# Kernel optimization log

Hardware: AMD Instinct MI355X
Metric: run time of the kernel (lower is better)

## Reference

```python
import jax, jax.numpy as jnp
import numpy as np

H = 128  # hidden size


def _gru_scan(xp, w_hh, b_hh):
    # xp: [T, B, 3H] precomputed input projections, PyTorch gate order (r, z, n)
    h0 = jnp.zeros((xp.shape[1], H), xp.dtype)
    def step(h, xt):
        g = h @ w_hh.T + b_hh
        xr, xz, xn = jnp.split(xt, 3, axis=-1)
        hr, hz, hn = jnp.split(g, 3, axis=-1)
        r = jax.nn.sigmoid(xr + hr)
        z = jax.nn.sigmoid(xz + hz)
        n = jnp.tanh(xn + r * hn)
        h = (1.0 - z) * n + z * h
        return h, h
    h_T, ys = jax.lax.scan(step, h0, xp)
    return h_T, ys


def _bidir_layer(x, wi_f, wh_f, bi_f, bh_f, wi_b, wh_b, bi_b, bh_b):
    # x: [T, B, D_in] time-major; returns concat outputs [T, B, 2H] and final hiddens
    h_f, y_f = _gru_scan(x @ wi_f.T + bi_f, wh_f, bh_f)
    h_b, y_b = _gru_scan(x[::-1] @ wi_b.T + bi_b, wh_b, bh_b)
    return jnp.concatenate([y_f, y_b[::-1]], axis=-1), h_f, h_b


def setup_inputs() -> dict:
    key = jax.random.key(0)
    ks = iter(jax.random.split(key, 40))
    scale = 1.0 / np.sqrt(H)
    def p(shape):
        return jax.random.normal(next(ks), shape, jnp.float32) * scale
    inp = {"x": jax.random.normal(next(ks), (512, 512, 4), jnp.float32)}
    for l, din in ((0, 4), (1, 2 * H)):
        for d in ("f", "b"):
            inp[f"w_ih_l{l}{d}"] = p((3 * H, din))
            inp[f"w_hh_l{l}{d}"] = p((3 * H, H))
            inp[f"b_ih_l{l}{d}"] = p((3 * H,))
            inp[f"b_hh_l{l}{d}"] = p((3 * H,))
    inp["fc1_w"] = p((H, 2 * H)); inp["fc1_b"] = p((H,))
    inp["fc2_w"] = p((2, H));     inp["fc2_b"] = p((2,))
    return inp


def reference(x, w_ih_l0f, w_hh_l0f, b_ih_l0f, b_hh_l0f,
              w_ih_l0b, w_hh_l0b, b_ih_l0b, b_hh_l0b,
              w_ih_l1f, w_hh_l1f, b_ih_l1f, b_hh_l1f,
              w_ih_l1b, w_hh_l1b, b_ih_l1b, b_hh_l1b,
              fc1_w, fc1_b, fc2_w, fc2_b):
    xt = jnp.transpose(x, (1, 0, 2))  # [T, B, F] time-major
    y0, _, _ = _bidir_layer(xt, w_ih_l0f, w_hh_l0f, b_ih_l0f, b_hh_l0f,
                            w_ih_l0b, w_hh_l0b, b_ih_l0b, b_hh_l0b)
    # dropout between layers is identity in eval mode
    _, h_f, h_b = _bidir_layer(y0, w_ih_l1f, w_hh_l1f, b_ih_l1f, b_hh_l1f,
                               w_ih_l1b, w_hh_l1b, b_ih_l1b, b_hh_l1b)
    h = jnp.concatenate([h_f, h_b], axis=-1)  # [B, 2H] = last-layer final hiddens, fwd then bwd
    h = jax.nn.relu(h @ fc1_w.T + fc1_b)
    return h @ fc2_w.T + fc2_b  # [B, num_classes]
```

## Files before the change

kernel.cpp:

```cpp
#include <hip/hip_runtime.h>
#include <stdint.h>


#define Tt 512
#define Bb 512
#define THREADS 512

using s16x8 = __attribute__((ext_vector_type(8))) short;
using f32x4 = __attribute__((ext_vector_type(4))) float;

#define MF(a, b, c) __builtin_amdgcn_mfma_f32_16x16x32_bf16((a), (b), (c), 0, 0, 0)

__device__ __forceinline__ unsigned short f2bf(float f) {
    union { float f; unsigned int u; } v; v.f = f;
    unsigned int u = v.u;
    u += 0x7fffu + ((u >> 16) & 1u);
    return (unsigned short)(u >> 16);
}
__device__ __forceinline__ float bf2f(unsigned short h) {
    union { unsigned int u; float f; } v; v.u = ((unsigned int)h) << 16;
    return v.f;
}

__device__ __forceinline__ float fsig(float x) {
    return __builtin_amdgcn_rcpf(1.0f + __expf(-x));
}
__device__ __forceinline__ float ftanh(float x) {
    return 2.0f * __builtin_amdgcn_rcpf(1.0f + __expf(-2.0f * x)) - 1.0f;
}

#define WG_BARRIER() asm volatile("s_waitcnt lgkmcnt(0)\n\ts_barrier" ::: "memory")

__global__ void w_prep(const float* __restrict__ wihf, const float* __restrict__ wihb,
                       const float* __restrict__ bihf, const float* __restrict__ bihb,
                       unsigned short* __restrict__ wcat, float* __restrict__ bcat)
{
    const int n = blockIdx.x;
    const int k = threadIdx.x;
    const float* src = (n < 384) ? &wihf[(size_t)n * 256] : &wihb[(size_t)(n - 384) * 256];
    wcat[(size_t)n * 256 + k] = f2bf(src[k]);
    if (k == 0) bcat[n] = (n < 384) ? bihf[n] : bihb[n - 384];
}

__global__ __launch_bounds__(THREADS) void l1_step(
    const unsigned short* __restrict__ y0,
    const unsigned short* __restrict__ wcat,
    const float* __restrict__ bcat,
    const unsigned short* __restrict__ gx_rd,
    unsigned short* __restrict__ gx_wr,
    const float* __restrict__ whh_f, const float* __restrict__ bhh_f,
    const float* __restrict__ whh_b, const float* __restrict__ bhh_b,
    float* __restrict__ hstate,
    int CT, int kgemm, int nscan, int first)
{
    const int bid  = blockIdx.x;
    const int tid  = threadIdx.x;
    const int wave = tid >> 6;
    const int lane = tid & 63;
    const int lcol = lane & 15;
    const int quad = lane >> 4;

    __shared__ __align__(16) unsigned short lA[128][136];
    __shared__ __align__(16) unsigned short lB[128][136];
    __shared__ __align__(16) unsigned short lds_h[2][16][136];

    if (bid >= nscan) {
        int gb = bid - nscan;
        const int nt = gb % 3;  gb /= 3;
        const int bt = gb & 3;  gb >>= 2;
        const int sl = gb % CT;
        const int dir = gb / CT;
        const int s  = kgemm * CT + sl;
        const int t  = dir ? (511 - s) : s;
        const int bb = bt << 7;

        const unsigned short* Abase = y0 + ((size_t)t * 512 + bb) * 256;
        const unsigned short* Bbase = wcat + ((size_t)dir * 384 + nt * 128) * 256;

        const int r0 = (wave >> 2) * 64;
        const int c0 = (wave & 3) * 32;

        f32x4 acc[4][2];
#pragma unroll
        for (int ti = 0; ti < 4; ++ti)
#pragma unroll
            for (int tj = 0; tj < 2; ++tj) acc[ti][tj] = {0.f, 0.f, 0.f, 0.f};

        const int rstg = tid >> 4;
        const int cstg = (tid & 15) * 8;

#pragma unroll
        for (int kh = 0; kh < 2; ++kh) {
            if (kh) __syncthreads();
#pragma unroll
            for (int it = 0; it < 4; ++it) {
                const int r = it * 32 + rstg;
                *(ulonglong2*)&lA[r][cstg] =
                    *(const ulonglong2*)&Abase[(size_t)r * 256 + kh * 128 + cstg];
                *(ulonglong2*)&lB[r][cstg] =
                    *(const ulonglong2*)&Bbase[(size_t)r * 256 + kh * 128 + cstg];
            }
            __syncthreads();

#pragma unroll
            for (int kk = 0; kk < 4; ++kk) {
                s16x8 af[4], bfv[2];
#pragma unroll
                for (int ti = 0; ti < 4; ++ti)
                    af[ti] = *(const s16x8*)&lA[r0 + ti * 16 + lcol][kk * 32 + quad * 8];
#pragma unroll
                for (int tj = 0; tj < 2; ++tj)
                    bfv[tj] = *(const s16x8*)&lB[c0 + tj * 16 + lcol][kk * 32 + quad * 8];
#pragma unroll
                for (int ti = 0; ti < 4; ++ti)
#pragma unroll
                    for (int tj = 0; tj < 2; ++tj)
                        acc[ti][tj] = MF(af[ti], bfv[tj], acc[ti][tj]);
            }
        }

        float bias[2];
#pragma unroll
        for (int tj = 0; tj < 2; ++tj)
            bias[tj] = bcat[dir * 384 + nt * 128 + c0 + tj * 16 + lcol];

        __syncthreads();

        unsigned short* lC = &lA[0][0];
#pragma unroll
        for (int ti = 0; ti < 4; ++ti)
#pragma unroll
            for (int tj = 0; tj < 2; ++tj) {
                const int col = c0 + tj * 16 + lcol;
#pragma unroll
                for (int i = 0; i < 4; ++i)
                    lC[(size_t)(r0 + ti * 16 + 4 * quad + i) * 136 + col] =
                        f2bf(acc[ti][tj][i] + bias[tj]);
            }
        __syncthreads();

        unsigned short* ob = gx_wr + ((size_t)(dir * CT + sl) * 512 + bb) * 384 + nt * 128;
#pragma unroll
        for (int it = 0; it < 4; ++it) {
            const int r = it * 32 + rstg;
            *(ulonglong2*)&ob[(size_t)r * 384 + cstg] =
                *(const ulonglong2*)&lC[(size_t)r * 136 + cstg];
        }
        return;
    }

    const int dir   = bid >> 5;
    const int chunk = bid & 31;
    const int b0    = chunk * 16;
    const int c     = 16 * wave + lcol;

    const float* whh = dir ? whh_b : whh_f;
    const float* bhh = dir ? bhh_b : bhh_f;

    const float bhr = bhh[c];
    const float bhz = bhh[128 + c];
    const float bhn = bhh[256 + c];

    s16x8 bh[3][4];
#pragma unroll
    for (int p = 0; p < 3; ++p) {
        const int nrow = p * 128 + c;
#pragma unroll
        for (int kk = 0; kk < 4; ++kk) {
            const float* src = &whh[(size_t)nrow * 128 + kk * 32 + quad * 8];
            s16x8 f;
#pragma unroll
            for (int j = 0; j < 8; ++j) f[j] = (short)f2bf(src[j]);
            bh[p][kk] = f;
        }
    }

    const unsigned short* gbase = gx_rd + (size_t)dir * CT * 512 * 384;
    auto loadGX = [&](unsigned short (&G)[12], int sl) {
        const unsigned short* gp = gbase + ((size_t)sl * 512 + b0 + 4 * quad) * 384;
#pragma unroll
        for (int g = 0; g < 3; ++g)
#pragma unroll
            for (int i = 0; i < 4; ++i)
                G[g * 4 + i] = gp[(size_t)i * 384 + g * 128 + c];
    };
    unsigned short G0[12], G1[12];
    loadGX(G0, 0);
    loadGX(G1, 1);

    float hreg[4];
    const int gb2 = tid >> 5;
    const int j0  = (tid & 31) * 4;
    if (first) {
#pragma unroll
        for (int i = 0; i < 4; ++i) hreg[i] = 0.f;
        ushort4 z4; z4.x = 0; z4.y = 0; z4.z = 0; z4.w = 0;
        *(ushort4*)&lds_h[0][gb2][j0] = z4;
    } else {
#pragma unroll
        for (int i = 0; i < 4; ++i)
            hreg[i] = hstate[(size_t)(b0 + 4 * quad + i) * 256 + dir * 128 + c];
        ushort4 hv;
        hv.x = f2bf(hstate[(size_t)(b0 + gb2) * 256 + dir * 128 + j0 + 0]);
        hv.y = f2bf(hstate[(size_t)(b0 + gb2) * 256 + dir * 128 + j0 + 1]);
        hv.z = f2bf(hstate[(size_t)(b0 + gb2) * 256 + dir * 128 + j0 + 2]);
        hv.w = f2bf(hstate[(size_t)(b0 + gb2) * 256 + dir * 128 + j0 + 3]);
        *(ushort4*)&lds_h[0][gb2][j0] = hv;
    }
    __syncthreads();

#define L1C_STEP(S, PAR, G)                                                    \
    do {                                                                       \
        const s16x8 a0 = *(const s16x8*)&lds_h[PAR][lcol][0  + quad * 8];      \
        const s16x8 a1 = *(const s16x8*)&lds_h[PAR][lcol][32 + quad * 8];      \
        const s16x8 a2 = *(const s16x8*)&lds_h[PAR][lcol][64 + quad * 8];      \
        const s16x8 a3 = *(const s16x8*)&lds_h[PAR][lcol][96 + quad * 8];      \
        f32x4 rA = {bhr, bhr, bhr, bhr}, rB = {0.f, 0.f, 0.f, 0.f};            \
        f32x4 zA = {bhz, bhz, bhz, bhz}, zB = {0.f, 0.f, 0.f, 0.f};            \
        f32x4 nA = {bhn, bhn, bhn, bhn}, nB = {0.f, 0.f, 0.f, 0.f};            \
        rA = MF(a0, bh[0][0], rA); zA = MF(a0, bh[1][0], zA);                  \
        nA = MF(a0, bh[2][0], nA);                                             \
        rB = MF(a1, bh[0][1], rB); zB = MF(a1, bh[1][1], zB);                  \
        nB = MF(a1, bh[2][1], nB);                                             \
        rA = MF(a2, bh[0][2], rA); zA = MF(a2, bh[1][2], zA);                  \
        nA = MF(a2, bh[2][2], nA);                                             \
        rB = MF(a3, bh[0][3], rB); zB = MF(a3, bh[1][3], zB);                  \
        nB = MF(a3, bh[2][3], nB);                                             \
        _Pragma("unroll")                                                      \
        for (int i = 0; i < 4; ++i) {                                          \
            const float r = fsig(rA[i] + rB[i] + bf2f(G[i]));                  \
            const float z = fsig(zA[i] + zB[i] + bf2f(G[4 + i]));              \
            const float n = ftanh(bf2f(G[8 + i]) + r * (nA[i] + nB[i]));       \
            hreg[i] = (1.0f - z) * n + z * hreg[i];                            \
            lds_h[PAR ^ 1][4 * quad + i][c] = f2bf(hreg[i]);                   \
        }                                                                      \
        if ((S) < CT - 2) {                                                    \
            loadGX(G, (S) + 2);                                                \
        } else if ((S) == CT - 1) {                                            \
            _Pragma("unroll")                                                  \
            for (int i = 0; i < 4; ++i)                                        \
                hstate[(size_t)(b0 + 4 * quad + i) * 256 + dir * 128 + c] =    \
                    hreg[i];                                                   \
        }                                                                      \
        WG_BARRIER();                                                          \
    } while (0)

    for (int sl = 0; sl < CT; sl += 2) {
        L1C_STEP(sl,     0, G0);
        L1C_STEP(sl + 1, 1, G1);
    }
#undef L1C_STEP
}

__global__ __launch_bounds__(THREADS, 1) void gru_l1(
    const unsigned short* __restrict__ y0,
    const float* __restrict__ wih_f, const float* __restrict__ whh_f,
    const float* __restrict__ bih_f, const float* __restrict__ bhh_f,
    const float* __restrict__ wih_b, const float* __restrict__ whh_b,
    const float* __restrict__ bih_b, const float* __restrict__ bhh_b,
    float* __restrict__ finals)
{
    const int tid  = threadIdx.x;
    const int wave = tid >> 6;
    const int lane = tid & 63;
    const int lcol = lane & 15;
    const int quad = lane >> 4;
    const int dir   = blockIdx.x >> 5;
    const int b0    = (blockIdx.x & 31) * 16;
    const int c     = 16 * wave + lcol;

    const float* wih = dir ? wih_b : wih_f;
    const float* whh = dir ? whh_b : whh_f;
    const float* bih = dir ? bih_b : bih_f;
    const float* bhh = dir ? bhh_b : bhh_f;

    __shared__ __align__(16) unsigned short lds_h[2][16][136];

    const float br  = bih[c]       + bhh[c];
    const float bz  = bih[128 + c] + bhh[128 + c];
    const float bnx = bih[256 + c];
    const float bnh = bhh[256 + c];

    s16x8 bh[3][4];
    s16x8 bx[3][8];
#pragma unroll
    for (int p = 0; p < 3; ++p) {
        const int nrow = p * 128 + c;
#pragma unroll
        for (int kk = 0; kk < 4; ++kk) {
            const float* src = &whh[(size_t)nrow * 128 + kk * 32 + quad * 8];
            s16x8 f;
#pragma unroll
            for (int j = 0; j < 8; ++j) f[j] = (short)f2bf(src[j]);
            bh[p][kk] = f;
        }
#pragma unroll
        for (int kk = 0; kk < 8; ++kk) {
            const float* src = &wih[(size_t)nrow * 256 + kk * 32 + quad * 8];
            s16x8 f;
#pragma unroll
            for (int j = 0; j < 8; ++j) f[j] = (short)f2bf(src[j]);
            bx[p][kk] = f;
        }
    }

    auto loadP = [&](s16x8 (&P)[8], int t) {
        const unsigned short* pb = y0 + ((size_t)t * Bb + b0 + lcol) * 256 + quad * 8;
#pragma unroll
        for (int kk = 0; kk < 8; ++kk) P[kk] = *(const s16x8*)(pb + kk * 32);
    };
    s16x8 P0[8], P1[8];
    loadP(P0, dir ? 511 : 0);
    loadP(P1, dir ? 510 : 1);

    f32x4 accr = {br, br, br, br};
    f32x4 accz = {bz, bz, bz, bz};
    f32x4 accnx = {bnx, bnx, bnx, bnx};
#pragma unroll
    for (int kk = 0; kk < 8; ++kk) {
        accr  = MF(P0[kk], bx[0][kk], accr);
        accz  = MF(P0[kk], bx[1][kk], accz);
        accnx = MF(P0[kk], bx[2][kk], accnx);
    }
    loadP(P0, dir ? 509 : 2);

    float hreg[4] = {0.f, 0.f, 0.f, 0.f};
    for (int idx = tid; idx < 2 * 16 * 136; idx += THREADS)
        ((unsigned short*)lds_h)[idx] = 0;
    __syncthreads();

#define L1_STEP(S, PAR, PN)                                                    \
    do {                                                                       \
        const s16x8 a0 = *(const s16x8*)&lds_h[PAR][lcol][0  + quad * 8];      \
        const s16x8 a1 = *(const s16x8*)&lds_h[PAR][lcol][32 + quad * 8];      \
        const s16x8 a2 = *(const s16x8*)&lds_h[PAR][lcol][64 + quad * 8];      \
        const s16x8 a3 = *(const s16x8*)&lds_h[PAR][lcol][96 + quad * 8];      \
        f32x4 acchn = {bnh, bnh, bnh, bnh};                                    \
        accr = MF(a0, bh[0][0], accr); accz = MF(a0, bh[1][0], accz);          \
        acchn = MF(a0, bh[2][0], acchn);                                       \
        accr = MF(a1, bh[0][1], accr); accz = MF(a1, bh[1][1], accz);          \
        acchn = MF(a1, bh[2][1], acchn);                                       \
        accr = MF(a2, bh[0][2], accr); accz = MF(a2, bh[1][2], accz);          \
        acchn = MF(a2, bh[2][2], acchn);                                       \
        accr = MF(a3, bh[0][3], accr); accz = MF(a3, bh[1][3], accz);          \
        acchn = MF(a3, bh[2][3], acchn);                                       \
        _Pragma("unroll")                                                      \
        for (int i = 0; i < 4; ++i) {                                          \
            const float r = fsig(accr[i]);                                     \
            const float z = fsig(accz[i]);                                     \
            const float n = ftanh(accnx[i] + r * acchn[i]);                    \
            hreg[i] = (1.0f - z) * n + z * hreg[i];                            \
            lds_h[PAR ^ 1][4 * quad + i][c] = f2bf(hreg[i]);                   \
        }                                                                      \
        if ((S) < 511) {                                                       \
            accr = {br, br, br, br}; accz = {bz, bz, bz, bz};                  \
            accnx = {bnx, bnx, bnx, bnx};                                      \
            _Pragma("unroll")                                                  \
            for (int kk = 0; kk < 8; ++kk) {                                   \
                accr  = MF(PN[kk], bx[0][kk], accr);                           \
                accz  = MF(PN[kk], bx[1][kk], accz);                           \
                accnx = MF(PN[kk], bx[2][kk], accnx);                          \
            }                                                                  \
            int sp = (S) + 3; if (sp > 511) sp = 511;                          \
            loadP(PN, dir ? (511 - sp) : sp);                                  \
        } else {                                                               \
            _Pragma("unroll")                                                  \
            for (int i = 0; i < 4; ++i)                                        \
                finals[(size_t)(b0 + 4 * quad + i) * 256 + dir * 128 + c] =    \
                    hreg[i];                                                   \
        }                                                                      \
        WG_BARRIER();                                                          \
    } while (0)

    for (int s = 0; s < Tt; s += 2) {
        L1_STEP(s,     0, P1);
        L1_STEP(s + 1, 1, P0);
    }
#undef L1_STEP
}

__global__ __launch_bounds__(THREADS, 1) void gru_l0(
    const float* __restrict__ x,
    const float* __restrict__ wih_f, const float* __restrict__ whh_f,
    const float* __restrict__ bih_f, const float* __restrict__ bhh_f,
    const float* __restrict__ wih_b, const float* __restrict__ whh_b,
    const float* __restrict__ bih_b, const float* __restrict__ bhh_b,
    unsigned short* __restrict__ y0)
{
    const int tid  = threadIdx.x;
    const int wave = tid >> 6;
    const int lane = tid & 63;
    const int lcol = lane & 15;
    const int quad = lane >> 4;
    const int dir   = blockIdx.x >> 5;
    const int b0    = (blockIdx.x & 31) * 16;
    const int c     = 16 * wave + lcol;

    const float* wih = dir ? wih_b : wih_f;
    const float* whh = dir ? whh_b : whh_f;
    const float* bih = dir ? bih_b : bih_f;
    const float* bhh = dir ? bhh_b : bhh_f;

    __shared__ __align__(16) unsigned short lds_h[2][16][136];

    const float brs  = bih[c]       + bhh[c];
    const float bzs  = bih[128 + c] + bhh[128 + c];
    const float bnxs = bih[256 + c];
    const float bnh  = bhh[256 + c];

    float wr[4], wz[4], wn[4];
#pragma unroll
    for (int f = 0; f < 4; ++f) {
        wr[f] = wih[(c)       * 4 + f];
        wz[f] = wih[(128 + c) * 4 + f];
        wn[f] = wih[(256 + c) * 4 + f];
    }

    s16x8 bh[3][4];
#pragma unroll
    for (int p = 0; p < 3; ++p) {
        const int nrow = p * 128 + c;
#pragma unroll
        for (int kk = 0; kk < 4; ++kk) {
            const float* src = &whh[(size_t)nrow * 128 + kk * 32 + quad * 8];
            s16x8 f;
#pragma unroll
            for (int j = 0; j < 8; ++j) f[j] = (short)f2bf(src[j]);
            bh[p][kk] = f;
        }
    }

    auto loadX = [&](float4 (&X)[4], int t) {
#pragma unroll
        for (int i = 0; i < 4; ++i)
            X[i] = *(const float4*)&x[((size_t)(b0 + 4 * quad + i) * Tt + t) * 4];
    };
    float4 X0[4], X1[4];
    loadX(X0, dir ? 511 : 0);
    loadX(X1, dir ? 510 : 1);

    float xpr[4], xpz[4], xpn[4];
#pragma unroll
    for (int i = 0; i < 4; ++i) {
        xpr[i] = brs  + X0[i].x * wr[0] + X0[i].y * wr[1] + X0[i].z * wr[2] + X0[i].w * wr[3];
        xpz[i] = bzs  + X0[i].x * wz[0] + X0[i].y * wz[1] + X0[i].z * wz[2] + X0[i].w * wz[3];
        xpn[i] = bnxs + X0[i].x * wn[0] + X0[i].y * wn[1] + X0[i].z * wn[2] + X0[i].w * wn[3];
    }
    loadX(X0, dir ? 509 : 2);

    float hreg[4] = {0.f, 0.f, 0.f, 0.f};
    for (int idx = tid; idx < 2 * 16 * 136; idx += THREADS)
        ((unsigned short*)lds_h)[idx] = 0;
    __syncthreads();

    const int orow = tid >> 5;
    const int oc4  = (tid & 31) * 4;

#define L0_STEP(S, PAR, XN)                                                    \
    do {                                                                       \
        const int t = dir ? (511 - (S)) : (S);                                 \
        const s16x8 a0 = *(const s16x8*)&lds_h[PAR][lcol][0  + quad * 8];      \
        const s16x8 a1 = *(const s16x8*)&lds_h[PAR][lcol][32 + quad * 8];      \
        const s16x8 a2 = *(const s16x8*)&lds_h[PAR][lcol][64 + quad * 8];      \
        const s16x8 a3 = *(const s16x8*)&lds_h[PAR][lcol][96 + quad * 8];      \
        f32x4 accr  = {xpr[0], xpr[1], xpr[2], xpr[3]};                        \
        f32x4 accz  = {xpz[0], xpz[1], xpz[2], xpz[3]};                        \
        f32x4 acchn = {bnh, bnh, bnh, bnh};                                    \
        accr = MF(a0, bh[0][0], accr); accz = MF(a0, bh[1][0], accz);          \
        acchn = MF(a0, bh[2][0], acchn);                                       \
        accr = MF(a1, bh[0][1], accr); accz = MF(a1, bh[1][1], accz);          \
        acchn = MF(a1, bh[2][1], acchn);                                       \
        accr = MF(a2, bh[0][2], accr); accz = MF(a2, bh[1][2], accz);          \
        acchn = MF(a2, bh[2][2], acchn);                                       \
        accr = MF(a3, bh[0][3], accr); accz = MF(a3, bh[1][3], accz);          \
        acchn = MF(a3, bh[2][3], acchn);                                       \
        _Pragma("unroll")                                                      \
        for (int i = 0; i < 4; ++i) {                                          \
            const float r = fsig(accr[i]);                                     \
            const float z = fsig(accz[i]);                                     \
            const float n = ftanh(xpn[i] + r * acchn[i]);                      \
            hreg[i] = (1.0f - z) * n + z * hreg[i];                            \
            lds_h[PAR ^ 1][4 * quad + i][c] = f2bf(hreg[i]);                   \
        }                                                                      \
        if ((S) < 511) {                                                       \
            _Pragma("unroll")                                                  \
            for (int i = 0; i < 4; ++i) {                                      \
                xpr[i] = brs  + XN[i].x * wr[0] + XN[i].y * wr[1]              \
                              + XN[i].z * wr[2] + XN[i].w * wr[3];             \
                xpz[i] = bzs  + XN[i].x * wz[0] + XN[i].y * wz[1]              \
                              + XN[i].z * wz[2] + XN[i].w * wz[3];             \
                xpn[i] = bnxs + XN[i].x * wn[0] + XN[i].y * wn[1]              \
                              + XN[i].z * wn[2] + XN[i].w * wn[3];             \
            }                                                                  \
            int sp = (S) + 3; if (sp > 511) sp = 511;                          \
            loadX(XN, dir ? (511 - sp) : sp);                                  \
        }                                                                      \
        WG_BARRIER();                                                          \
        {                                                                      \
            const ushort4 hv4 = *(const ushort4*)&lds_h[PAR ^ 1][orow][oc4];   \
            *(ushort4*)&y0[((size_t)t * Bb + b0 + orow) * 256 + dir * 128 +    \
                           oc4] = hv4;                                         \
        }                                                                      \
    } while (0)

    for (int s = 0; s < Tt; s += 2) {
        L0_STEP(s,     0, X1);
        L0_STEP(s + 1, 1, X0);
    }
#undef L0_STEP
}

__global__ __launch_bounds__(128) void fc_head(
    const float* __restrict__ finals,
    const float* __restrict__ fc1w, const float* __restrict__ fc1b,
    const float* __restrict__ fc2w, const float* __restrict__ fc2b,
    float* __restrict__ out)
{
    __shared__ float s_in[256];
    __shared__ float s_h1[128];
    const int b = blockIdx.x, tid = threadIdx.x;
    s_in[tid]       = finals[(size_t)b * 256 + tid];
    s_in[tid + 128] = finals[(size_t)b * 256 + 128 + tid];
    __syncthreads();
    float acc = fc1b[tid];
    const float* wrow = &fc1w[tid * 256];
#pragma unroll 8
    for (int i = 0; i < 256; ++i) acc += s_in[i] * wrow[i];
    s_h1[tid] = fmaxf(acc, 0.0f);
    __syncthreads();
    if (tid < 2) {
        float a = fc2b[tid];
        const float* w2 = &fc2w[tid * 128];
#pragma unroll 8
        for (int i = 0; i < 128; ++i) a += s_h1[i] * w2[i];
        out[b * 2 + tid] = a;
    }
}

extern "C" void kernel_launch(void* const* d_in, const int* in_sizes, int n_in,
                              void* d_out, int out_size, void* d_ws, size_t ws_size,
                              hipStream_t stream) {
    const float* x      = (const float*)d_in[0];
    const float* wih0f  = (const float*)d_in[1];
    const float* whh0f  = (const float*)d_in[2];
    const float* bih0f  = (const float*)d_in[3];
    const float* bhh0f  = (const float*)d_in[4];
    const float* wih0b  = (const float*)d_in[5];
    const float* whh0b  = (const float*)d_in[6];
    const float* bih0b  = (const float*)d_in[7];
    const float* bhh0b  = (const float*)d_in[8];
    const float* wih1f  = (const float*)d_in[9];
    const float* whh1f  = (const float*)d_in[10];
    const float* bih1f  = (const float*)d_in[11];
    const float* bhh1f  = (const float*)d_in[12];
    const float* wih1b  = (const float*)d_in[13];
    const float* whh1b  = (const float*)d_in[14];
    const float* bih1b  = (const float*)d_in[15];
    const float* bhh1b  = (const float*)d_in[16];
    const float* fc1w   = (const float*)d_in[17];
    const float* fc1b   = (const float*)d_in[18];
    const float* fc2w   = (const float*)d_in[19];
    const float* fc2b   = (const float*)d_in[20];

    const size_t Y0SZ = 134217728ull;
    const size_t HSSZ = 524288ull;
    const size_t WCSZ = 393216ull;
    const size_t BCSZ = 3072ull;
    const size_t GX_PER_SL = 786432ull;
    const size_t BASE = Y0SZ + HSSZ + WCSZ + BCSZ;

    unsigned short* y0 = (unsigned short*)d_ws;
    float*  hstate = (float*)((char*)d_ws + Y0SZ);
    unsigned short* wcat = (unsigned short*)((char*)d_ws + Y0SZ + HSSZ);
    float*  bcat   = (float*)((char*)d_ws + Y0SZ + HSSZ + WCSZ);
    unsigned short* gx0 = (unsigned short*)((char*)d_ws + BASE);
    float* out = (float*)d_out;

    const int cts[6] = {128, 64, 32, 16, 8, 4};
    int CT = 0, fused = 0;
    for (int i = 0; i < 6; ++i)
        if (BASE + 2ull * cts[i] * GX_PER_SL <= ws_size) { CT = cts[i]; fused = 1; break; }
    if (!CT)
        for (int i = 0; i < 6; ++i)
            if (BASE + (size_t)cts[i] * GX_PER_SL <= ws_size) { CT = cts[i]; break; }

    if (CT > 0) {
        unsigned short* gxb[2];
        gxb[0] = gx0;
        gxb[1] = fused ? (unsigned short*)((char*)gx0 + (size_t)CT * GX_PER_SL) : gx0;

        w_prep<<<dim3(768), dim3(256), 0, stream>>>(wih1f, wih1b, bih1f, bih1b, wcat, bcat);
        gru_l0<<<dim3(64), dim3(THREADS), 0, stream>>>(
            x, wih0f, whh0f, bih0f, bhh0f, wih0b, whh0b, bih0b, bhh0b, y0);
        const int n = Tt / CT;
        if (fused) {
            l1_step<<<dim3(24 * CT), dim3(THREADS), 0, stream>>>(
                y0, wcat, bcat, gxb[0], gxb[0],
                whh1f, bhh1f, whh1b, bhh1b, hstate, CT, 0, 0, 1);
            for (int k = 0; k < n; ++k) {
                const int ng = (k + 1 < n) ? 24 * CT : 0;
                l1_step<<<dim3(64 + ng), dim3(THREADS), 0, stream>>>(
                    y0, wcat, bcat, gxb[k & 1], gxb[(k + 1) & 1],
                    whh1f, bhh1f, whh1b, bhh1b, hstate, CT, k + 1, 64, (k == 0) ? 1 : 0);
            }
        } else {
            for (int k = 0; k < n; ++k) {
                l1_step<<<dim3(24 * CT), dim3(THREADS), 0, stream>>>(
                    y0, wcat, bcat, gxb[0], gxb[0],
                    whh1f, bhh1f, whh1b, bhh1b, hstate, CT, k, 0, 1);
                l1_step<<<dim3(64), dim3(THREADS), 0, stream>>>(
                    y0, wcat, bcat, gxb[0], gxb[0],
                    whh1f, bhh1f, whh1b, bhh1b, hstate, CT, 0, 64, (k == 0) ? 1 : 0);
            }
        }
        fc_head<<<dim3(Bb), dim3(128), 0, stream>>>(hstate, fc1w, fc1b, fc2w, fc2b, out);
    } else {
        float* finals = (float*)((char*)d_ws + Y0SZ);
        gru_l0<<<dim3(64), dim3(THREADS), 0, stream>>>(
            x, wih0f, whh0f, bih0f, bhh0f, wih0b, whh0b, bih0b, bhh0b, y0);
        gru_l1<<<dim3(64), dim3(THREADS), 0, stream>>>(
            y0, wih1f, whh1f, bih1f, bhh1f, wih1b, whh1b, bih1b, bhh1b, finals);
        fc_head<<<dim3(Bb), dim3(128), 0, stream>>>(finals, fc1w, fc1b, fc2w, fc2b, out);
    }
}
```

Before: 1.214 ms.

## Split layer-0 GRU across 256 blocks with four batch rows each

The layer-0 recurrent kernel now gives each block 4 batch rows instead of 16 and launches 256 blocks instead of 64, spreading the work over more compute units. The 16x16 MFMA still runs at full size, so three quarters of its rows are zero padding. Lane shuffles move each row's gate results to the quad that owns it, so each thread updates a single hidden value. Output stores become scalar 16-bit writes. The serial time-step chain per block is unchanged, so the extra parallelism may not shorten it, and the shuffles add latency to every step.

After: 1.150 ms. -5.3%, faster.

```diff
diff --git a/kernel.cpp b/kernel.cpp
--- a/kernel.cpp
+++ b/kernel.cpp
@@ -392,8 +392,9 @@
     const int lane = tid & 63;
     const int lcol = lane & 15;
     const int quad = lane >> 4;
-    const int dir   = blockIdx.x >> 5;
-    const int b0    = (blockIdx.x & 31) * 16;
+    const int dir   = blockIdx.x >> 7;
+    const int chunk = blockIdx.x & 127;
+    const int b0    = chunk * 4;
     const int c     = 16 * wave + lcol;
 
     const float* wih = dir ? wih_b : wih_f;
@@ -433,7 +434,7 @@
     auto loadX = [&](float4 (&X)[4], int t) {
 #pragma unroll
         for (int i = 0; i < 4; ++i)
-            X[i] = *(const float4*)&x[((size_t)(b0 + 4 * quad + i) * Tt + t) * 4];
+            X[i] = *(const float4*)&x[((size_t)(b0 + i) * Tt + t) * 4];
     };
     float4 X0[4], X1[4];
     loadX(X0, dir ? 511 : 0);
@@ -448,13 +449,13 @@
     }
     loadX(X0, dir ? 509 : 2);
 
-    float hreg[4] = {0.f, 0.f, 0.f, 0.f};
+    float hmine = 0.f;
     for (int idx = tid; idx < 2 * 16 * 136; idx += THREADS)
         ((unsigned short*)lds_h)[idx] = 0;
     __syncthreads();
 
-    const int orow = tid >> 5;
-    const int oc4  = (tid & 31) * 4;
+    const int orow = tid >> 7;
+    const int ocol = tid & 127;
 
 #define L0_STEP(S, PAR, XN)                                                    \
     do {                                                                       \
@@ -474,13 +475,24 @@
         acchn = MF(a2, bh[2][2], acchn);                                       \
         accr = MF(a3, bh[0][3], accr); accz = MF(a3, bh[1][3], accz);          \
         acchn = MF(a3, bh[2][3], acchn);                                       \
-        _Pragma("unroll")                                                      \
-        for (int i = 0; i < 4; ++i) {                                          \
-            const float r = fsig(accr[i]);                                     \
-            const float z = fsig(accz[i]);                                     \
-            const float n = ftanh(xpn[i] + r * acchn[i]);                      \
-            hreg[i] = (1.0f - z) * n + z * hreg[i];                            \
-            lds_h[PAR ^ 1][4 * quad + i][c] = f2bf(hreg[i]);                   \
+         \
+        float rr0 = __shfl(accr[0], lcol), rr1 = __shfl(accr[1], lcol);        \
+        float rr2 = __shfl(accr[2], lcol), rr3 = __shfl(accr[3], lcol);        \
+        float zz0 = __shfl(accz[0], lcol), zz1 = __shfl(accz[1], lcol);        \
+        float zz2 = __shfl(accz[2], lcol), zz3 = __shfl(accz[3], lcol);        \
+        float hh0 = __shfl(acchn[0], lcol), hh1 = __shfl(acchn[1], lcol);      \
+        float hh2 = __shfl(acchn[2], lcol), hh3 = __shfl(acchn[3], lcol);      \
+        const float pr = quad == 0 ? rr0 : quad == 1 ? rr1 : quad == 2 ? rr2 : rr3; \
+        const float pz = quad == 0 ? zz0 : quad == 1 ? zz1 : quad == 2 ? zz2 : zz3; \
+        const float ph = quad == 0 ? hh0 : quad == 1 ? hh1 : quad == 2 ? hh2 : hh3; \
+        const float pn = quad == 0 ? xpn[0] : quad == 1 ? xpn[1]               \
+                       : quad == 2 ? xpn[2] : xpn[3];                          \
+        {                                                                      \
+            const float r = fsig(pr);                                          \
+            const float z = fsig(pz);                                          \
+            const float n = ftanh(pn + r * ph);                                \
+            hmine = (1.0f - z) * n + z * hmine;                                \
+            lds_h[PAR ^ 1][quad][c] = f2bf(hmine);                             \
         }                                                                      \
         if ((S) < 511) {                                                       \
             _Pragma("unroll")                                                  \
@@ -497,9 +509,9 @@
         }                                                                      \
         WG_BARRIER();                                                          \
         {                                                                      \
-            const ushort4 hv4 = *(const ushort4*)&lds_h[PAR ^ 1][orow][oc4];   \
-            *(ushort4*)&y0[((size_t)t * Bb + b0 + orow) * 256 + dir * 128 +    \
-                           oc4] = hv4;                                         \
+                        \
+            y0[((size_t)t * Bb + b0 + orow) * 256 + dir * 128 + ocol] =        \
+                lds_h[PAR ^ 1][orow][ocol];                                    \
         }                                                                      \
     } while (0)
 
@@ -590,7 +602,7 @@
         gxb[1] = fused ? (unsigned short*)((char*)gx0 + (size_t)CT * GX_PER_SL) : gx0;
 
         w_prep<<<dim3(768), dim3(256), 0, stream>>>(wih1f, wih1b, bih1f, bih1b, wcat, bcat);
-        gru_l0<<<dim3(64), dim3(THREADS), 0, stream>>>(
+        gru_l0<<<dim3(256), dim3(THREADS), 0, stream>>>(
             x, wih0f, whh0f, bih0f, bhh0f, wih0b, whh0b, bih0b, bhh0b, y0);
         const int n = Tt / CT;
         if (fused) {
@@ -616,7 +628,7 @@
         fc_head<<<dim3(Bb), dim3(128), 0, stream>>>(hstate, fc1w, fc1b, fc2w, fc2b, out);
     } else {
         float* finals = (float*)((char*)d_ws + Y0SZ);
-        gru_l0<<<dim3(64), dim3(THREADS), 0, stream>>>(
+        gru_l0<<<dim3(256), dim3(THREADS), 0, stream>>>(
             x, wih0f, whh0f, bih0f, bhh0f, wih0b, whh0b, bih0b, bhh0b, y0);
         gru_l1<<<dim3(64), dim3(THREADS), 0, stream>>>(
             y0, wih1f, whh1f, bih1f, bhh1f, wih1b, whh1b, bih1b, bhh1b, finals);
```
